# Kernel tuning notes

Hardware: AMD Instinct MI355X
Metric: run time of the kernel (lower is better)

## Reference

```python
import jax, jax.numpy as jnp
import numpy as np

TOP_K = 2


def setup_inputs() -> dict:
    key = jax.random.key(0)
    kx, kw = jax.random.split(key)
    B, S, D, E = 4, 4096, 2048, 64
    x = jax.random.normal(kx, (B, S, D), dtype=jnp.float32)
    W = jax.random.normal(kw, (E, D), dtype=jnp.float32) * 0.02  # router weight [E, D]
    return {"x": x, "W": W}


def reference(x, W):
    B, S, D = x.shape
    E = W.shape[0]
    x_flat = x.reshape(-1, D)                      # [T, D], T = B*S
    router_logits = jnp.einsum('td,ed->te', x_flat, W)  # [T, E]
    router_probs = jax.nn.softmax(router_logits, axis=-1)
    expert_weights, expert_indices = jax.lax.top_k(router_probs, TOP_K)  # [T, K]
    expert_weights = expert_weights / jnp.sum(expert_weights, axis=-1, keepdims=True)
    expert_indices = expert_indices.reshape(B, S, TOP_K)
    expert_weights = expert_weights.reshape(B, S, TOP_K)
    # aux load-balance loss: sum((mean usage - 1/E)^2)
    expert_usage = jnp.mean(router_probs, axis=0)  # [E]
    aux_loss = jnp.sum((expert_usage - 1.0 / E) ** 2)
    return expert_indices, expert_weights, aux_loss
```

## Files before the change

kernel.cpp:

```cpp
#include <hip/hip_runtime.h>
#include <math.h>

#define T_TOK 16384
#define DDIM  2048
#define NE    64
#define NPLANE (NE * DDIM)
#define NBLK  512

typedef __attribute__((ext_vector_type(8))) short short8;
typedef __attribute__((ext_vector_type(4))) float floatx4;

union Frag8 { unsigned short u[8]; short8 v; };

__device__ __forceinline__ unsigned int bf16_rne_bits(float x) {
    unsigned int u = __builtin_bit_cast(unsigned int, x);
    return (u + 0x7fffu + ((u >> 16) & 1u)) & 0xffff0000u;
}

__global__ void wsplit_kernel(const float* __restrict__ W,
                              unsigned short* __restrict__ wh,
                              unsigned short* __restrict__ wm,
                              unsigned short* __restrict__ wl) {
    int i = blockIdx.x * 256 + threadIdx.x;
    float w = W[i];
    unsigned int hb = bf16_rne_bits(w);
    float r  = w - __builtin_bit_cast(float, hb);
    unsigned int mb = bf16_rne_bits(r);
    float r2 = r - __builtin_bit_cast(float, mb);
    unsigned int lb = bf16_rne_bits(r2);
    wh[i] = (unsigned short)(hb >> 16);
    wm[i] = (unsigned short)(mb >> 16);
    wl[i] = (unsigned short)(lb >> 16);
}

__global__ __launch_bounds__(512, 4)
void router_main(const float* __restrict__ x,
                 const unsigned short* __restrict__ wh,
                 const unsigned short* __restrict__ wm,
                 const unsigned short* __restrict__ wl,
                 float* __restrict__ out, float* __restrict__ usage_part) {
    __shared__ float lg[8 * 2048];
    __shared__ float ured[8][NE];

    const int tid  = threadIdx.x;
    const int lane = tid & 63;
    const int wv   = __builtin_amdgcn_readfirstlane(tid >> 6);
    const int cl   = lane & 15;
    const int q    = lane >> 4;
    const int t0   = blockIdx.x * 32;

    const float* xa = x + (size_t)(t0 + cl) * DDIM + wv * 256 + q * 8;
    const size_t bb = (size_t)cl * DDIM + wv * 256 + q * 8;

    floatx4 acc[2][4];
#pragma unroll
    for (int mt = 0; mt < 2; ++mt)
#pragma unroll
        for (int nt = 0; nt < 4; ++nt)
            acc[mt][nt] = (floatx4){0.f, 0.f, 0.f, 0.f};

#pragma unroll
    for (int c = 0; c < 8; ++c) {
        const int ko = c * 32;

        uint4 cb[4][3];
#pragma unroll
        for (int nt = 0; nt < 4; ++nt) {
            const size_t o = bb + (size_t)nt * 16 * DDIM + ko;
            cb[nt][0] = *(const uint4*)(wh + o);
            cb[nt][1] = *(const uint4*)(wm + o);
            cb[nt][2] = *(const uint4*)(wl + o);
        }

        short8 Ah[2], Am[2], Al[2];
#pragma unroll
        for (int mt = 0; mt < 2; ++mt) {
            const float* ap = xa + (size_t)mt * 16 * DDIM + ko;
            float4 a0 = *(const float4*)(ap);
            float4 a1 = *(const float4*)(ap + 4);
            float f[8] = {a0.x, a0.y, a0.z, a0.w, a1.x, a1.y, a1.z, a1.w};
            Frag8 fh, fm, fl;
#pragma unroll
            for (int j = 0; j < 8; ++j) {
                unsigned int ub = __builtin_bit_cast(unsigned int, f[j]);
                unsigned int hb = ub & 0xffff0000u;
                float r = f[j] - __builtin_bit_cast(float, hb);
                unsigned int rb = __builtin_bit_cast(unsigned int, r);
                unsigned int mb = rb & 0xffff0000u;
                float r2 = r - __builtin_bit_cast(float, mb);
                unsigned int lb = __builtin_bit_cast(unsigned int, r2);
                fh.u[j] = (unsigned short)(hb >> 16);
                fm.u[j] = (unsigned short)(mb >> 16);
                fl.u[j] = (unsigned short)(lb >> 16);
            }
            Ah[mt] = fh.v; Am[mt] = fm.v; Al[mt] = fl.v;
        }

#pragma unroll
        for (int mt = 0; mt < 2; ++mt)
#pragma unroll
            for (int nt = 0; nt < 4; ++nt) {
                short8 Bh = __builtin_bit_cast(short8, cb[nt][0]);
                short8 Bm = __builtin_bit_cast(short8, cb[nt][1]);
                short8 Bl = __builtin_bit_cast(short8, cb[nt][2]);
                floatx4 a = acc[mt][nt];
                a = __builtin_amdgcn_mfma_f32_16x16x32_bf16(Ah[mt], Bh, a, 0, 0, 0);
                a = __builtin_amdgcn_mfma_f32_16x16x32_bf16(Ah[mt], Bm, a, 0, 0, 0);
                a = __builtin_amdgcn_mfma_f32_16x16x32_bf16(Am[mt], Bh, a, 0, 0, 0);
                a = __builtin_amdgcn_mfma_f32_16x16x32_bf16(Am[mt], Bm, a, 0, 0, 0);
                a = __builtin_amdgcn_mfma_f32_16x16x32_bf16(Ah[mt], Bl, a, 0, 0, 0);
                a = __builtin_amdgcn_mfma_f32_16x16x32_bf16(Al[mt], Bh, a, 0, 0, 0);
                acc[mt][nt] = a;
            }
    }

#pragma unroll
    for (int mt = 0; mt < 2; ++mt)
#pragma unroll
        for (int nt = 0; nt < 4; ++nt)
#pragma unroll
            for (int r = 0; r < 4; ++r)
                lg[wv * 2048 + (mt * 16 + q * 4 + r) * 64 + nt * 16 + cl]
                    = acc[mt][nt][r];
    __syncthreads();

    float usage_acc = 0.f;
#pragma unroll 1
    for (int j = 0; j < 4; ++j) {
        const int tl = wv * 4 + j;
        const int t  = t0 + tl;
        float l = (((lg[0 * 2048 + tl * 64 + lane] + lg[1 * 2048 + tl * 64 + lane]) +
                    (lg[2 * 2048 + tl * 64 + lane] + lg[3 * 2048 + tl * 64 + lane])) +
                   ((lg[4 * 2048 + tl * 64 + lane] + lg[5 * 2048 + tl * 64 + lane]) +
                    (lg[6 * 2048 + tl * 64 + lane] + lg[7 * 2048 + tl * 64 + lane])));

        float v1 = l; int i1 = lane;
#pragma unroll
        for (int off = 32; off >= 1; off >>= 1) {
            float ov = __shfl_xor(v1, off, 64);
            int   oi = __shfl_xor(i1, off, 64);
            if (ov > v1 || (ov == v1 && oi < i1)) { v1 = ov; i1 = oi; }
        }
        float lm = (lane == i1) ? -INFINITY : l;
        float v2 = lm; int i2 = lane;
#pragma unroll
        for (int off = 32; off >= 1; off >>= 1) {
            float ov = __shfl_xor(v2, off, 64);
            int   oi = __shfl_xor(i2, off, 64);
            if (ov > v2 || (ov == v2 && oi < i2)) { v2 = ov; i2 = oi; }
        }

        float p = expf(l - v1);
        float s = p;
#pragma unroll
        for (int off = 32; off >= 1; off >>= 1) s += __shfl_xor(s, off, 64);

        float e2  = expf(v2 - v1);
        float rcp = 1.0f / (1.0f + e2);
        usage_acc += p / s;

        if (lane == 0) {
            out[(size_t)t * 2 + 0]         = (float)i1;
            out[(size_t)t * 2 + 1]         = (float)i2;
            out[32768 + (size_t)t * 2 + 0] = rcp;
            out[32768 + (size_t)t * 2 + 1] = e2 * rcp;
        }
    }

    ured[wv][lane] = usage_acc;
    __syncthreads();
    if (wv == 0) {
        float s = ((ured[0][lane] + ured[1][lane]) + (ured[2][lane] + ured[3][lane])) +
                  ((ured[4][lane] + ured[5][lane]) + (ured[6][lane] + ured[7][lane]));
        usage_part[(size_t)blockIdx.x * 64 + lane] = s;
    }
}

__global__ __launch_bounds__(1024)
void router_aux(const float* __restrict__ usage_part, float* __restrict__ out) {
    __shared__ float red[16][NE];
    const int tid = threadIdx.x;
    const int e   = tid & 63;
    const int g   = tid >> 6;
    float s = 0.f;
#pragma unroll
    for (int i = 0; i < NBLK / 16; ++i)
        s += usage_part[(size_t)(g * (NBLK / 16) + i) * 64 + e];
    red[g][e] = s;
    __syncthreads();
    if (g == 0) {
        float tot = 0.f;
#pragma unroll
        for (int i = 0; i < 16; ++i) tot += red[i][e];
        float u = tot * (1.0f / 16384.0f) - (1.0f / 64.0f);
        float sq = u * u;
#pragma unroll
        for (int off = 32; off >= 1; off >>= 1) sq += __shfl_xor(sq, off, 64);
        if (e == 0) out[65536] = sq;
    }
}

extern "C" void kernel_launch(void* const* d_in, const int* in_sizes, int n_in,
                              void* d_out, int out_size, void* d_ws, size_t ws_size,
                              hipStream_t stream) {
    const float* x = (const float*)d_in[0];
    const float* W = (const float*)d_in[1];
    float* out     = (float*)d_out;

    unsigned short* ws_h = (unsigned short*)d_ws;
    unsigned short* ws_m = ws_h + NPLANE;
    unsigned short* ws_l = ws_m + NPLANE;
    float* upart         = (float*)(ws_l + NPLANE);

    wsplit_kernel<<<dim3(NPLANE / 256), dim3(256), 0, stream>>>(W, ws_h, ws_m, ws_l);
    router_main<<<dim3(NBLK), dim3(512), 0, stream>>>(x, ws_h, ws_m, ws_l, out, upart);
    router_aux<<<dim3(1), dim3(1024), 0, stream>>>(upart, out);
}
```

Measured before the change: 243.8 us.

## Stream x and W splits through LDS ring via async global_load_lds pipeline

```diff
diff --git a/kernel.cpp b/kernel.cpp
--- a/kernel.cpp
+++ b/kernel.cpp
@@ -5,7 +5,8 @@
 #define DDIM  2048
 #define NE    64
 #define NPLANE (NE * DDIM)
-#define NBLK  512
+#define NBLK  256
+#define DRING 6
 
 typedef __attribute__((ext_vector_type(8))) short short8;
 typedef __attribute__((ext_vector_type(4))) float floatx4;
@@ -15,6 +16,12 @@
 __device__ __forceinline__ unsigned int bf16_rne_bits(float x) {
     unsigned int u = __builtin_bit_cast(unsigned int, x);
     return (u + 0x7fffu + ((u >> 16) & 1u)) & 0xffff0000u;
+}
+
+__device__ __forceinline__ void dma16(const void* g, void* lds) {
+    __builtin_amdgcn_global_load_lds(
+        (const __attribute__((address_space(1))) unsigned int*)g,
+        (__attribute__((address_space(3))) unsigned int*)lds, 16, 0, 0);
 }
 
 __global__ void wsplit_kernel(const float* __restrict__ W,
@@ -33,106 +40,126 @@
     wl[i] = (unsigned short)(lb >> 16);
 }
 
-__global__ __launch_bounds__(512, 4)
+__global__ __launch_bounds__(512, 2)
 void router_main(const float* __restrict__ x,
-                 const unsigned short* __restrict__ wh,
-                 const unsigned short* __restrict__ wm,
-                 const unsigned short* __restrict__ wl,
+                 const unsigned short* __restrict__ whp,
+                 const unsigned short* __restrict__ wmp,
+                 const unsigned short* __restrict__ wlp,
                  float* __restrict__ out, float* __restrict__ usage_part) {
-    __shared__ float lg[8 * 2048];
-    __shared__ float ured[8][NE];
+    __shared__ float          ringA[DRING * 2048];
+    __shared__ unsigned short ringB[DRING * 6144];
+    __shared__ float          lg[64 * 64];
+    __shared__ float          ured[8][NE];
 
     const int tid  = threadIdx.x;
     const int lane = tid & 63;
     const int wv   = __builtin_amdgcn_readfirstlane(tid >> 6);
+    const int tg   = wv >> 1;
+    const int eh   = wv & 1;
     const int cl   = lane & 15;
     const int q    = lane >> 4;
-    const int t0   = blockIdx.x * 32;
-
-    const float* xa = x + (size_t)(t0 + cl) * DDIM + wv * 256 + q * 8;
-    const size_t bb = (size_t)cl * DDIM + wv * 256 + q * 8;
-
-    floatx4 acc[2][4];
-#pragma unroll
-    for (int mt = 0; mt < 2; ++mt)
-#pragma unroll
-        for (int nt = 0; nt < 4; ++nt)
-            acc[mt][nt] = (floatx4){0.f, 0.f, 0.f, 0.f};
-
-#pragma unroll
-    for (int c = 0; c < 8; ++c) {
-        const int ko = c * 32;
-
-        uint4 cb[4][3];
-#pragma unroll
-        for (int nt = 0; nt < 4; ++nt) {
-            const size_t o = bb + (size_t)nt * 16 * DDIM + ko;
-            cb[nt][0] = *(const uint4*)(wh + o);
-            cb[nt][1] = *(const uint4*)(wm + o);
-            cb[nt][2] = *(const uint4*)(wl + o);
-        }
-
-        short8 Ah[2], Am[2], Al[2];
-#pragma unroll
-        for (int mt = 0; mt < 2; ++mt) {
-            const float* ap = xa + (size_t)mt * 16 * DDIM + ko;
-            float4 a0 = *(const float4*)(ap);
-            float4 a1 = *(const float4*)(ap + 4);
-            float f[8] = {a0.x, a0.y, a0.z, a0.w, a1.x, a1.y, a1.z, a1.w};
-            Frag8 fh, fm, fl;
-#pragma unroll
-            for (int j = 0; j < 8; ++j) {
-                unsigned int ub = __builtin_bit_cast(unsigned int, f[j]);
-                unsigned int hb = ub & 0xffff0000u;
-                float r = f[j] - __builtin_bit_cast(float, hb);
-                unsigned int rb = __builtin_bit_cast(unsigned int, r);
-                unsigned int mb = rb & 0xffff0000u;
-                float r2 = r - __builtin_bit_cast(float, mb);
-                unsigned int lb = __builtin_bit_cast(unsigned int, r2);
-                fh.u[j] = (unsigned short)(hb >> 16);
-                fm.u[j] = (unsigned short)(mb >> 16);
-                fl.u[j] = (unsigned short)(lb >> 16);
+    const int t0   = blockIdx.x * 64;
+
+    const int swcol = ((((lane & 7) * 16) ^ ((lane >> 3) << 4)) >> 2);
+    const int ai    = (wv >= 4) ? (wv - 4) * 2 : 0;
+    const float* asrc0 = x + (size_t)(t0 + ai * 8 + (lane >> 3)) * DDIM + swcol;
+    const float* asrc1 = asrc0 + (size_t)8 * DDIM;
+    const unsigned short* bsrc0 = whp + (size_t)lane * DDIM + wv * 8;
+    const unsigned short* bsrc1 = wmp + (size_t)lane * DDIM + wv * 8;
+    const unsigned short* bsrc2 = wlp + (size_t)lane * DDIM + wv * 8;
+
+    floatx4 acc[2];
+    acc[0] = (floatx4){0.f, 0.f, 0.f, 0.f};
+    acc[1] = (floatx4){0.f, 0.f, 0.f, 0.f};
+
+#pragma unroll
+    for (int s = 0; s < 5; ++s) {
+        if (wv < 4) {
+            dma16(bsrc0 + s * 32, (void*)(ringB + s * 6144 + 0 * 2048 + wv * 512));
+            dma16(bsrc1 + s * 32, (void*)(ringB + s * 6144 + 1 * 2048 + wv * 512));
+            dma16(bsrc2 + s * 32, (void*)(ringB + s * 6144 + 2 * 2048 + wv * 512));
+        } else {
+            dma16(asrc0 + s * 32, (void*)(ringA + s * 2048 + (ai + 0) * 256));
+            dma16(asrc1 + s * 32, (void*)(ringA + s * 2048 + (ai + 1) * 256));
+        }
+    }
+
+    int rs = 0, ws = 5;
+#pragma unroll 1
+    for (int c = 0; c < 64; ++c) {
+        if (wv < 4) { asm volatile("s_waitcnt vmcnt(12)" ::: "memory"); }
+        else        { asm volatile("s_waitcnt vmcnt(8)"  ::: "memory"); }
+        __builtin_amdgcn_s_barrier();
+        __builtin_amdgcn_sched_barrier(0);
+
+        {
+            int kd = c + 5; if (kd > 63) kd = 63;
+            if (wv < 4) {
+                dma16(bsrc0 + kd * 32, (void*)(ringB + ws * 6144 + 0 * 2048 + wv * 512));
+                dma16(bsrc1 + kd * 32, (void*)(ringB + ws * 6144 + 1 * 2048 + wv * 512));
+                dma16(bsrc2 + kd * 32, (void*)(ringB + ws * 6144 + 2 * 2048 + wv * 512));
+            } else {
+                dma16(asrc0 + kd * 32, (void*)(ringA + ws * 2048 + (ai + 0) * 256));
+                dma16(asrc1 + kd * 32, (void*)(ringA + ws * 2048 + (ai + 1) * 256));
             }
-            Ah[mt] = fh.v; Am[mt] = fm.v; Al[mt] = fl.v;
-        }
-
-#pragma unroll
-        for (int mt = 0; mt < 2; ++mt)
-#pragma unroll
-            for (int nt = 0; nt < 4; ++nt) {
-                short8 Bh = __builtin_bit_cast(short8, cb[nt][0]);
-                short8 Bm = __builtin_bit_cast(short8, cb[nt][1]);
-                short8 Bl = __builtin_bit_cast(short8, cb[nt][2]);
-                floatx4 a = acc[mt][nt];
-                a = __builtin_amdgcn_mfma_f32_16x16x32_bf16(Ah[mt], Bh, a, 0, 0, 0);
-                a = __builtin_amdgcn_mfma_f32_16x16x32_bf16(Ah[mt], Bm, a, 0, 0, 0);
-                a = __builtin_amdgcn_mfma_f32_16x16x32_bf16(Am[mt], Bh, a, 0, 0, 0);
-                a = __builtin_amdgcn_mfma_f32_16x16x32_bf16(Am[mt], Bm, a, 0, 0, 0);
-                a = __builtin_amdgcn_mfma_f32_16x16x32_bf16(Ah[mt], Bl, a, 0, 0, 0);
-                a = __builtin_amdgcn_mfma_f32_16x16x32_bf16(Al[mt], Bh, a, 0, 0, 0);
-                acc[mt][nt] = a;
-            }
-    }
-
-#pragma unroll
-    for (int mt = 0; mt < 2; ++mt)
-#pragma unroll
-        for (int nt = 0; nt < 4; ++nt)
-#pragma unroll
-            for (int r = 0; r < 4; ++r)
-                lg[wv * 2048 + (mt * 16 + q * 4 + r) * 64 + nt * 16 + cl]
-                    = acc[mt][nt][r];
+        }
+
+        const float* Arow = ringA + rs * 2048 + (tg * 16 + cl) * 32;
+        const int x0 = ((q * 32)      ^ ((cl & 7) << 4)) >> 2;
+        const int x1 = ((q * 32 + 16) ^ ((cl & 7) << 4)) >> 2;
+        float4 a0 = *(const float4*)(Arow + x0);
+        float4 a1 = *(const float4*)(Arow + x1);
+        float f[8] = {a0.x, a0.y, a0.z, a0.w, a1.x, a1.y, a1.z, a1.w};
+        Frag8 fh, fm, fl;
+#pragma unroll
+        for (int j = 0; j < 8; ++j) {
+            unsigned int ub = __builtin_bit_cast(unsigned int, f[j]);
+            unsigned int hb = ub & 0xffff0000u;
+            float r = f[j] - __builtin_bit_cast(float, hb);
+            unsigned int rb = __builtin_bit_cast(unsigned int, r);
+            unsigned int mb = rb & 0xffff0000u;
+            float r2 = r - __builtin_bit_cast(float, mb);
+            unsigned int lb = __builtin_bit_cast(unsigned int, r2);
+            fh.u[j] = (unsigned short)(hb >> 16);
+            fm.u[j] = (unsigned short)(mb >> 16);
+            fl.u[j] = (unsigned short)(lb >> 16);
+        }
+        short8 Ah = fh.v, Am = fm.v, Al = fl.v;
+
+#pragma unroll
+        for (int nt = 0; nt < 2; ++nt) {
+            const unsigned short* bp =
+                ringB + rs * 6144 + q * 512 + (eh * 32 + nt * 16 + cl) * 8;
+            short8 Bh = __builtin_bit_cast(short8, *(const uint4*)(bp));
+            short8 Bm = __builtin_bit_cast(short8, *(const uint4*)(bp + 2048));
+            short8 Bl = __builtin_bit_cast(short8, *(const uint4*)(bp + 4096));
+            floatx4 a = acc[nt];
+            a = __builtin_amdgcn_mfma_f32_16x16x32_bf16(Ah, Bh, a, 0, 0, 0);
+            a = __builtin_amdgcn_mfma_f32_16x16x32_bf16(Ah, Bm, a, 0, 0, 0);
+            a = __builtin_amdgcn_mfma_f32_16x16x32_bf16(Am, Bh, a, 0, 0, 0);
+            a = __builtin_amdgcn_mfma_f32_16x16x32_bf16(Am, Bm, a, 0, 0, 0);
+            a = __builtin_amdgcn_mfma_f32_16x16x32_bf16(Ah, Bl, a, 0, 0, 0);
+            a = __builtin_amdgcn_mfma_f32_16x16x32_bf16(Al, Bh, a, 0, 0, 0);
+            acc[nt] = a;
+        }
+
+        rs = (rs == DRING - 1) ? 0 : rs + 1;
+        ws = (ws == DRING - 1) ? 0 : ws + 1;
+    }
+
+#pragma unroll
+    for (int nt = 0; nt < 2; ++nt)
+#pragma unroll
+        for (int r = 0; r < 4; ++r)
+            lg[(tg * 16 + q * 4 + r) * 64 + eh * 32 + nt * 16 + cl] = acc[nt][r];
     __syncthreads();
 
     float usage_acc = 0.f;
 #pragma unroll 1
-    for (int j = 0; j < 4; ++j) {
-        const int tl = wv * 4 + j;
+    for (int j = 0; j < 8; ++j) {
+        const int tl = wv * 8 + j;
         const int t  = t0 + tl;
-        float l = (((lg[0 * 2048 + tl * 64 + lane] + lg[1 * 2048 + tl * 64 + lane]) +
-                    (lg[2 * 2048 + tl * 64 + lane] + lg[3 * 2048 + tl * 64 + lane])) +
-                   ((lg[4 * 2048 + tl * 64 + lane] + lg[5 * 2048 + tl * 64 + lane]) +
-                    (lg[6 * 2048 + tl * 64 + lane] + lg[7 * 2048 + tl * 64 + lane])));
+        float l = lg[tl * 64 + lane];
 
         float v1 = l; int i1 = lane;
 #pragma unroll
```

Result: slower. 269.2 us (+10.4%).
